# Optimization experiments

Hardware: AMD Instinct MI355X
Metric: run time of the kernel (lower is better)

## Reference

```python
import jax, jax.numpy as jnp
import numpy as np

ALPHA = 0.2          # LeakyReLU negative slope
NEG_BIG = -9e15      # mask value from the original code


def setup_inputs() -> dict:
    key = jax.random.key(0)
    k1, k2, k3, k4, k5 = jax.random.split(key, 5)
    N, Fin, Fout, C = 8192, 2048, 256, 8
    x = jax.random.normal(k1, (N, Fin), dtype=jnp.float32)
    # xavier_uniform-ish scale for params
    W = jax.random.normal(k2, (C, Fin, Fout), dtype=jnp.float32) / np.sqrt(Fin).astype(np.float32)
    a = jax.random.normal(k3, (2 * Fout, 1), dtype=jnp.float32) / np.sqrt(2 * Fout).astype(np.float32)
    cam_ids = jax.random.randint(k4, (N,), 0, C, dtype=jnp.int32)
    adj = jax.random.randint(k5, (N, N), 0, 2, dtype=jnp.int32)
    return {"x": x, "W": W, "a": a, "cam_ids": cam_ids, "adj": adj}


def reference(x, W, a, cam_ids, adj):
    N = x.shape[0]
    Fout = W.shape[-1]
    # per-node camera-specific projection: h[i] = x[i] @ W[cam_ids[i]]
    # compute all-camera projections (N, C, Fout) then gather per node;
    # avoids materializing W[cam_ids] of shape (N, Fin, Fout)
    hs = jnp.einsum('nd,cdo->nco', x, W)                       # (N, C, Fout)
    h = jnp.take_along_axis(hs, cam_ids[:, None, None], axis=1)[:, 0, :]  # (N, Fout)
    # e_ij = leakyrelu([h_i, h_j] @ a) = leakyrelu(h_i.a1 + h_j.a2)
    a1 = a[:Fout, 0]
    a2 = a[Fout:, 0]
    e = jax.nn.leaky_relu((h @ a1)[:, None] + (h @ a2)[None, :], ALPHA)  # (N, N)
    att = jnp.where(adj > 0, e, jnp.float32(NEG_BIG))
    att = jax.nn.softmax(att, axis=1)
    # dropout is identity at eval (p applied only in training)
    h_prime = att @ h                                          # (N, Fout)
    return jax.nn.elu(h_prime)                                 # concat=True -> ELU
```

## Files before the change

### kernel.cpp

```cpp
#include <hip/hip_runtime.h>

#define NR 8192
#define FIN 2048
#define FOUT 256
#define ALPHA 0.2f
#define NTMAX 136

typedef float f32x4 __attribute__((ext_vector_type(4)));
typedef float f32x16 __attribute__((ext_vector_type(16)));
typedef int i32x4 __attribute__((ext_vector_type(4)));
typedef unsigned int u32x4 __attribute__((ext_vector_type(4)));
typedef unsigned short u16x4 __attribute__((ext_vector_type(4)));
typedef unsigned short u16x8 __attribute__((ext_vector_type(8)));
typedef __bf16 bf16x8 __attribute__((ext_vector_type(8)));
typedef _Float16 f16x8 __attribute__((ext_vector_type(8)));
typedef _Float16 f16x4 __attribute__((ext_vector_type(4)));

__device__ __forceinline__ unsigned short f2bf(float f){
  unsigned u = __float_as_uint(f);
  return (unsigned short)((u + 0x7fffu + ((u >> 16) & 1u)) >> 16);
}
__device__ __forceinline__ float bf2f(unsigned short b){
  return __uint_as_float(((unsigned)b) << 16);
}

__device__ __forceinline__ void gload16(const void* gptr, void* lptr){
  __builtin_amdgcn_global_load_lds(
      (const __attribute__((address_space(1))) unsigned int*)gptr,
      (__attribute__((address_space(3))) unsigned int*)lptr, 16, 0, 0);
}

__global__ void k_bucket(const int* __restrict__ cam, int* __restrict__ rowlist,
                         int* __restrict__ tileCam, int* __restrict__ prows){
  __shared__ int cnt[256][8];
  __shared__ int base[8];
  __shared__ int scnt[8];
  __shared__ int tstart[9];
  __shared__ int tcL[NTMAX], tlocL[NTMAX];
  int t = threadIdx.x;
  int loc[8];
  #pragma unroll
  for (int c = 0; c < 8; c++) loc[c] = 0;
  for (int k = 0; k < 32; k++){ int n = t*32 + k; loc[cam[n] & 7]++; }
  #pragma unroll
  for (int c = 0; c < 8; c++) cnt[t][c] = loc[c];
  __syncthreads();
  if (t < 8){
    int s = 0;
    for (int i = 0; i < 256; i++){ int v = cnt[i][t]; cnt[i][t] = s; s += v; }
    scnt[t] = s;
  }
  __syncthreads();
  if (t == 0){
    int s = 0;
    for (int c = 0; c < 8; c++){ base[c] = s; s += scnt[c]; }
    int ts = 0;
    for (int c = 0; c < 8; c++){ tstart[c] = ts; ts += (scnt[c] + 63) >> 6; }
    tstart[8] = ts;
  }
  __syncthreads();
  int off[8];
  #pragma unroll
  for (int c = 0; c < 8; c++) off[c] = base[c] + cnt[t][c];
  for (int k = 0; k < 32; k++){
    int n = t*32 + k; int c = cam[n] & 7;
    rowlist[off[c]++] = n;
  }
  __syncthreads();
  if (t < NTMAX){
    int tc = -1, tl = 0;
    if (t < tstart[8]){
      for (int c = 0; c < 8; c++)
        if (t >= tstart[c] && t < tstart[c+1]){ tc = c; tl = t - tstart[c]; }
    }
    tcL[t] = tc; tlocL[t] = tl;
    tileCam[t] = tc;
  }
  __syncthreads();
  for (int s = t; s < NTMAX*64; s += 256){
    int tile = s >> 6;
    int c = tcL[tile];
    int v = -1;
    if (c >= 0){
      int li = tlocL[tile]*64 + (s & 63);
      if (li < scnt[c]) v = rowlist[base[c] + li];
    }
    prows[s] = v;
  }
}

__global__ __launch_bounds__(256) void k_wth(const float* __restrict__ W,
                                             _Float16* __restrict__ WhT){
  __shared__ _Float16 tl[64][72];
  int t = threadIdx.x;
  int k0 = blockIdx.x*64, n0 = blockIdx.y*64, c = blockIdx.z;
  {
    int kk = t >> 2, nq = (t & 3)*16;
    const float* src = W + ((size_t)c*FIN + k0 + kk)*FOUT + n0 + nq;
    #pragma unroll
    for (int q = 0; q < 4; q++){
      f32x4 v = *(const f32x4*)(src + q*4);
      #pragma unroll
      for (int e = 0; e < 4; e++) tl[nq + q*4 + e][kk] = (_Float16)v[e];
    }
  }
  __syncthreads();
  {
    int nn = t >> 2, kq = (t & 3)*16;
    union { u32x4 v[2]; _Float16 s[16]; } buf;
    #pragma unroll
    for (int e = 0; e < 16; e++) buf.s[e] = tl[nn][kq + e];
    u32x4* dst = (u32x4*)(WhT + ((size_t)c*FOUT + n0 + nn)*FIN + k0 + kq);
    dst[0] = buf.v[0]; dst[1] = buf.v[1];
  }
}

__global__ __launch_bounds__(256) void k_gmm(const float* __restrict__ x,
    const _Float16* __restrict__ WhT, const int* __restrict__ tileCam,
    const int* __restrict__ prows, float* __restrict__ partial, int klen){
  __shared__ _Float16 ab[2][10240];
  __shared__ int rows[64];
  __shared__ int growL[64];
  int tile = blockIdx.x;
  int cam = tileCam[tile];
  if (cam < 0) return;
  int t = threadIdx.x;
  if (t < 64){ int r = prows[tile*64 + t]; rows[t] = r; growL[t] = (r < 0) ? 0 : r; }
  __syncthreads();
  int ks = blockIdx.y;
  int k0 = ks * klen;
  int lane = t & 63, w = t >> 6;
  int wr = w >> 1, wc = w & 1;
  int rA = ((t >> 6) & 1)*32 + (t & 31);
  int koffA = (t >> 7)*16 + ((t >> 5) & 1)*8;
  const float* srcA = x + (size_t)growL[rA]*FIN + k0 + koffA;
  const _Float16* srcB[4];
  #pragma unroll
  for (int q = 0; q < 4; q++){
    int c2 = q*256 + t;
    int colg = ((c2 >> 6) & 7)*32 + (t & 31);
    srcB[q] = WhT + ((size_t)cam*FOUT + colg)*FIN + k0
            + (c2 >> 9)*16 + ((t >> 5) & 1)*8;
  }
  f32x16 acc[4];
  #pragma unroll
  for (int nb = 0; nb < 4; nb++)
    #pragma unroll
    for (int r = 0; r < 16; r++) acc[nb][r] = 0.f;

  int nsteps = klen >> 5;
  int cur = 0;
  {
    f32x4 a0 = *(const f32x4*)srcA;
    f32x4 a1 = *(const f32x4*)(srcA + 4);
    #pragma unroll
    for (int q = 0; q < 4; q++) gload16(srcB[q], &ab[0][2048 + (q*256 + t)*8]);
    f16x8 hv;
    #pragma unroll
    for (int e = 0; e < 4; e++){ hv[e] = (_Float16)a0[e]; hv[4+e] = (_Float16)a1[e]; }
    *(f16x8*)&ab[0][t*8] = hv;
  }
  __syncthreads();
  for (int s = 0; s < nsteps; s++){
    bool have = (s + 1 < nsteps);
    int adv = have ? (s + 1)*32 : 0;
    f32x4 na0 = *(const f32x4*)(srcA + adv);
    f32x4 na1 = *(const f32x4*)(srcA + adv + 4);
    if (have){
      #pragma unroll
      for (int q = 0; q < 4; q++)
        gload16(srcB[q] + adv, &ab[cur ^ 1][2048 + (q*256 + t)*8]);
    }
    const _Float16* base = ab[cur];
    f16x8 af[2]; f16x8 bfr[2][4];
    #pragma unroll
    for (int kk = 0; kk < 2; kk++){
      af[kk] = *(const f16x8*)(base + ((kk*2 + wr)*64 + lane)*8);
      #pragma unroll
      for (int nb = 0; nb < 4; nb++)
        bfr[kk][nb] = *(const f16x8*)(base + 2048 + ((kk*8 + wc*4 + nb)*64 + lane)*8);
    }
    #pragma unroll
    for (int kk = 0; kk < 2; kk++)
      #pragma unroll
      for (int nb = 0; nb < 4; nb++)
        acc[nb] = __builtin_amdgcn_mfma_f32_32x32x16_f16(af[kk], bfr[kk][nb], acc[nb], 0, 0, 0);
    if (have){
      f16x8 hv;
      #pragma unroll
      for (int e = 0; e < 4; e++){ hv[e] = (_Float16)na0[e]; hv[4+e] = (_Float16)na1[e]; }
      *(f16x8*)&ab[cur ^ 1][t*8] = hv;
    }
    __syncthreads();
    cur ^= 1;
  }
  int colb = wc*128;
  #pragma unroll
  for (int nb = 0; nb < 4; nb++){
    #pragma unroll
    for (int r = 0; r < 16; r++){
      int rowl = wr*32 + (r & 3) + 8*(r >> 2) + 4*(lane >> 5);
      int grow = rows[rowl];
      if (grow >= 0)
        partial[((size_t)ks*NR + grow)*FOUT + colb + nb*32 + (lane & 31)] = acc[nb][r];
    }
  }
}

__global__ __launch_bounds__(256) void k_hsum(const float* __restrict__ partial,
    const float* __restrict__ a, unsigned short* __restrict__ hbf,
    float* __restrict__ s1, float* __restrict__ s2, float* __restrict__ bm,
    int ksplit){
  __shared__ float a1l[FOUT], a2l[FOUT];
  __shared__ float smax[4];
  int t = threadIdx.x;
  a1l[t] = a[t]; a2l[t] = a[FOUT + t];
  __syncthreads();
  int w = t >> 6, lane = t & 63;
  int row = blockIdx.x*4 + w;
  f32x4 s; s[0] = s[1] = s[2] = s[3] = 0.f;
  for (int ks = 0; ks < ksplit; ks++)
    s += *(const f32x4*)(partial + ((size_t)ks*NR + row)*FOUT + lane*4);
  u16x4 pk;
  #pragma unroll
  for (int e = 0; e < 4; e++) pk[e] = f2bf(s[e]);
  *(u16x4*)(hbf + (size_t)row*FOUT + lane*4) = pk;
  f32x4 a1v = *(const f32x4*)&a1l[lane*4];
  f32x4 a2v = *(const f32x4*)&a2l[lane*4];
  float p1 = 0.f, p2 = 0.f;
  #pragma unroll
  for (int e = 0; e < 4; e++){ p1 = fmaf(s[e], a1v[e], p1); p2 = fmaf(s[e], a2v[e], p2); }
  #pragma unroll
  for (int off = 32; off > 0; off >>= 1){
    p1 += __shfl_xor(p1, off);
    p2 += __shfl_xor(p2, off);
  }
  if (lane == 0){ s1[row] = p1; s2[row] = p2; smax[w] = p2; }
  __syncthreads();
  if (t == 0)
    bm[blockIdx.x] = fmaxf(fmaxf(smax[0], smax[1]), fmaxf(smax[2], smax[3]));
}

__global__ void k_transpose(const unsigned short* __restrict__ in,
                            unsigned short* __restrict__ out){
  __shared__ unsigned short tl[64][72];
  int t = threadIdx.x;
  int j0 = blockIdx.x*64, c0 = blockIdx.y*64;
  {
    int jj = t >> 2, cq = (t & 3)*16;
    union { u32x4 v[2]; unsigned short s[16]; } buf;
    const u32x4* src = (const u32x4*)(in + (size_t)(j0 + jj)*FOUT + c0 + cq);
    buf.v[0] = src[0]; buf.v[1] = src[1];
    #pragma unroll
    for (int k = 0; k < 16; k++) tl[cq + k][jj] = buf.s[k];
  }
  __syncthreads();
  {
    int cc = t >> 2, jq = (t & 3)*16;
    union { u32x4 v[2]; unsigned short s[16]; } buf;
    #pragma unroll
    for (int k = 0; k < 16; k++) buf.s[k] = tl[cc][jq + k];
    u32x4* dst = (u32x4*)(out + (size_t)(c0 + cc)*NR + j0 + jq);
    dst[0] = buf.v[0]; dst[1] = buf.v[1];
  }
}

__global__ __launch_bounds__(512) void k_flash(const int* __restrict__ adj,
    const float* __restrict__ s1g, const float* __restrict__ s2g,
    const float* __restrict__ bm, const unsigned short* __restrict__ hT,
    float* __restrict__ hp, float* __restrict__ Dp, int jchunks){
  __shared__ unsigned short pl[64][72];
  __shared__ float s1l[64], ml[64], Dl[64], red[8];
  int t = threadIdx.x;
  int i0 = blockIdx.x*64;
  int jc = blockIdx.y;
  int nj = NR / jchunks;
  int jbase = jc * nj;
  int w = t >> 6, lane = t & 63;
  {
    float v = -3.0e38f;
    for (int k = t; k < NR/4; k += 512) v = fmaxf(v, bm[k]);
    #pragma unroll
    for (int off = 32; off > 0; off >>= 1) v = fmaxf(v, __shfl_xor(v, off));
    if (lane == 0) red[w] = v;
  }
  __syncthreads();
  if (t == 0){
    float v = red[0];
    #pragma unroll
    for (int k = 1; k < 8; k++) v = fmaxf(v, red[k]);
    red[0] = v;
  }
  __syncthreads();
  float maxS2 = red[0];
  if (t < 64){
    float sv = s1g[i0 + t];
    s1l[t] = sv;
    float mm = sv + maxS2;
    ml[t] = fmaxf(mm, ALPHA*mm);
  }
  __syncthreads();
  int il = t >> 3, tj = t & 7;
  float s1i = s1l[il], mi = ml[il];
  float Dacc = 0.f;
  f32x16 acc0, acc1;
  #pragma unroll
  for (int k = 0; k < 16; k++){ acc0[k] = 0.f; acc1[k] = 0.f; }
  const unsigned short* hTw = hT + (size_t)(w*32 + (lane & 31))*NR;
  const int* arow = adj + (size_t)(i0 + il)*NR + jbase + tj*8;
  i32x4 ad0 = __builtin_nontemporal_load((const i32x4*)arow);
  i32x4 ad1 = __builtin_nontemporal_load(((const i32x4*)arow) + 1);
  f32x4 s20 = *(const f32x4*)(s2g + jbase + tj*8);
  f32x4 s21 = *(const f32x4*)(s2g + jbase + tj*8 + 4);
  for (int jt = 0; jt < nj; jt += 64){
    int j0 = jbase + jt;
    i32x4 c0 = ad0, c1 = ad1;
    f32x4 t0 = s20, t1 = s21;
    if (jt + 64 < nj){
      arow += 64;
      ad0 = __builtin_nontemporal_load((const i32x4*)arow);
      ad1 = __builtin_nontemporal_load(((const i32x4*)arow) + 1);
      s20 = *(const f32x4*)(s2g + j0 + 64 + tj*8);
      s21 = *(const f32x4*)(s2g + j0 + 64 + tj*8 + 4);
    }
    u16x8 pu;
    float Dloc = 0.f;
    #pragma unroll
    for (int e = 0; e < 4; e++){
      float e0 = s1i + t0[e]; e0 = fmaxf(e0, ALPHA*e0);
      float p0 = (c0[e] > 0) ? __expf(e0 - mi) : 0.f;
      unsigned short b0 = f2bf(p0); pu[e] = b0; Dloc += bf2f(b0);
      float e1 = s1i + t1[e]; e1 = fmaxf(e1, ALPHA*e1);
      float p1 = (c1[e] > 0) ? __expf(e1 - mi) : 0.f;
      unsigned short b1 = f2bf(p1); pu[e + 4] = b1; Dloc += bf2f(b1);
    }
    Dacc += Dloc;
    bf16x8 bfr[4];
    #pragma unroll
    for (int ks = 0; ks < 4; ks++){
      int koff = ks*16 + (lane >> 5)*8;
      bfr[ks] = *(const bf16x8*)(hTw + j0 + koff);
    }
    *(u16x8*)&pl[il][tj*8] = pu;
    __syncthreads();
    #pragma unroll
    for (int ks = 0; ks < 4; ks++){
      int koff = ks*16 + (lane >> 5)*8;
      bf16x8 a0 = *(const bf16x8*)&pl[lane & 31][koff];
      acc0 = __builtin_amdgcn_mfma_f32_32x32x16_bf16(a0, bfr[ks], acc0, 0, 0, 0);
      bf16x8 a1 = *(const bf16x8*)&pl[32 + (lane & 31)][koff];
      acc1 = __builtin_amdgcn_mfma_f32_32x32x16_bf16(a1, bfr[ks], acc1, 0, 0, 0);
    }
    __syncthreads();
  }
  Dacc += __shfl_xor(Dacc, 1);
  Dacc += __shfl_xor(Dacc, 2);
  Dacc += __shfl_xor(Dacc, 4);
  if (tj == 0) Dl[il] = Dacc;
  __syncthreads();
  if (t < 64) Dp[(size_t)jc*NR + i0 + t] = Dl[t];
  float* hpb = hp + (size_t)jc*NR*FOUT;
  int col = w*32 + (lane & 31);
  #pragma unroll
  for (int r = 0; r < 16; r++){
    int rowl = (r & 3) + 8*(r >> 2) + 4*(lane >> 5);
    hpb[(size_t)(i0 + rowl)*FOUT + col] = acc0[r];
    hpb[(size_t)(i0 + 32 + rowl)*FOUT + col] = acc1[r];
  }
}

__global__ void k_final(const float* __restrict__ hp, const float* __restrict__ Dp,
                        float* __restrict__ out, int jchunks){
  int g = blockIdx.x*256 + threadIdx.x;
  int i = g >> 6, cg = (g & 63)*4;
  f32x4 s; s[0] = s[1] = s[2] = s[3] = 0.f;
  float D = 0.f;
  for (int jc = 0; jc < jchunks; jc++){
    f32x4 v = *(const f32x4*)(hp + ((size_t)jc*NR + i)*FOUT + cg);
    s += v;
    D += Dp[(size_t)jc*NR + i];
  }
  float inv = (D > 0.f) ? 1.f / D : 0.f;
  f32x4 o;
  #pragma unroll
  for (int e = 0; e < 4; e++){
    float v = s[e]*inv;
    o[e] = (v > 0.f) ? v : expm1f(v);
  }
  *(f32x4*)(out + (size_t)i*FOUT + cg) = o;
}

extern "C" void kernel_launch(void* const* d_in, const int* in_sizes, int n_in,
                              void* d_out, int out_size, void* d_ws, size_t ws_size,
                              hipStream_t stream){
  (void)in_sizes; (void)n_in; (void)out_size;
  const float* x   = (const float*)d_in[0];
  const float* W   = (const float*)d_in[1];
  const float* a   = (const float*)d_in[2];
  const int*   cam = (const int*)d_in[3];
  const int*   adj = (const int*)d_in[4];
  float* out = (float*)d_out;
  char* ws = (char*)d_ws;

  int KS = 4, JC = 4;
  for (;;){
    size_t need = 0;
    need += (size_t)NR*4 + 256;
    need += (size_t)NTMAX*4 + 256;
    need += (size_t)NTMAX*64*4 + 256;
    need += (size_t)8*FIN*FOUT*2 + 256;
    need += (size_t)NR*FOUT*2 + 256;
    need += (size_t)NR*FOUT*2 + 256;
    need += (size_t)NR*4*2 + 512;
    need += (size_t)(NR/4)*4 + 256;
    need += (size_t)JC*NR*4 + 256;
    size_t sh1 = (size_t)KS*NR*FOUT*4;
    size_t sh2 = (size_t)JC*NR*FOUT*4;
    need += (sh1 > sh2 ? sh1 : sh2) + 256;
    if (need <= ws_size || (KS == 1 && JC == 1)) break;
    if (KS > 1) KS >>= 1;
    if (JC > 1) JC >>= 1;
  }

  size_t off = 0;
  auto alloc = [&](size_t b) -> void* {
    void* p = ws + off; off = (off + b + 255) & ~(size_t)255; return p;
  };
  int* rowlist  = (int*)alloc((size_t)NR*4);
  int* tileCam  = (int*)alloc((size_t)NTMAX*4);
  int* prows    = (int*)alloc((size_t)NTMAX*64*4);
  _Float16* WhT = (_Float16*)alloc((size_t)8*FIN*FOUT*2);
  unsigned short* hbf = (unsigned short*)alloc((size_t)NR*FOUT*2);
  unsigned short* hT  = (unsigned short*)alloc((size_t)NR*FOUT*2);
  float* s1 = (float*)alloc((size_t)NR*4);
  float* s2 = (float*)alloc((size_t)NR*4);
  float* bm = (float*)alloc((size_t)(NR/4)*4);
  float* Dp = (float*)alloc((size_t)JC*NR*4);
  size_t sh1 = (size_t)KS*NR*FOUT*4;
  size_t sh2 = (size_t)JC*NR*FOUT*4;
  void* shared = alloc(sh1 > sh2 ? sh1 : sh2);
  float* partial = (float*)shared;
  float* hp      = (float*)shared;

  int klen = FIN / KS;

  hipLaunchKernelGGL(k_bucket, dim3(1), dim3(256), 0, stream,
                     cam, rowlist, tileCam, prows);
  hipLaunchKernelGGL(k_wth, dim3(FIN/64, FOUT/64, 8), dim3(256), 0, stream, W, WhT);
  hipLaunchKernelGGL(k_gmm, dim3(NTMAX, KS), dim3(256), 0, stream,
                     x, WhT, tileCam, prows, partial, klen);
  hipLaunchKernelGGL(k_hsum, dim3(NR/4), dim3(256), 0, stream,
                     partial, a, hbf, s1, s2, bm, KS);
  hipLaunchKernelGGL(k_transpose, dim3(NR/64, FOUT/64), dim3(256), 0, stream, hbf, hT);
  hipLaunchKernelGGL(k_flash, dim3(NR/64, JC), dim3(512), 0, stream,
                     adj, s1, s2, bm, hT, hp, Dp, JC);
  hipLaunchKernelGGL(k_final, dim3((NR*FOUT/4)/256), dim3(256), 0, stream,
                     hp, Dp, out, JC);
}
```

Measured before the change: 236.3 us.

## Fuse hsum with transpose, flash with final via cooperative grid sync

Several kernels are merged. Row summation now writes the transposed bf16 h directly, which drops the separate transpose kernel and the hbf buffer. The bucket kernel writes prows directly instead of going through a rowlist pass. Flash attention and the final normalisation/ELU run in one cooperative kernel separated by a grid sync, with JC fixed at 2 and a fallback to separate launches. Split sizes become compile-time constants; the trade-off is only 128 blocks for hsumT and the cost of the grid barrier.

Result: slower. 271.8 us (+15.0%).

```diff
diff --git a/kernel.cpp b/kernel.cpp
--- a/kernel.cpp
+++ b/kernel.cpp
@@ -1,10 +1,18 @@
 #include <hip/hip_runtime.h>
+#include <hip/hip_cooperative_groups.h>
+
+namespace cg = cooperative_groups;
 
 #define NR 8192
 #define FIN 2048
 #define FOUT 256
 #define ALPHA 0.2f
 #define NTMAX 136
+#define KS 4
+#define KLEN 512
+#define NSTEPS 16
+#define JC 2
+#define NJ 4096
 
 typedef float f32x4 __attribute__((ext_vector_type(4)));
 typedef float f32x16 __attribute__((ext_vector_type(16)));
@@ -14,7 +22,6 @@
 typedef unsigned short u16x8 __attribute__((ext_vector_type(8)));
 typedef __bf16 bf16x8 __attribute__((ext_vector_type(8)));
 typedef _Float16 f16x8 __attribute__((ext_vector_type(8)));
-typedef _Float16 f16x4 __attribute__((ext_vector_type(4)));
 
 __device__ __forceinline__ unsigned short f2bf(float f){
   unsigned u = __float_as_uint(f);
@@ -23,25 +30,54 @@
 __device__ __forceinline__ float bf2f(unsigned short b){
   return __uint_as_float(((unsigned)b) << 16);
 }
-
 __device__ __forceinline__ void gload16(const void* gptr, void* lptr){
   __builtin_amdgcn_global_load_lds(
       (const __attribute__((address_space(1))) unsigned int*)gptr,
       (__attribute__((address_space(3))) unsigned int*)lptr, 16, 0, 0);
 }
 
-__global__ void k_bucket(const int* __restrict__ cam, int* __restrict__ rowlist,
-                         int* __restrict__ tileCam, int* __restrict__ prows){
-  __shared__ int cnt[256][8];
-  __shared__ int base[8];
-  __shared__ int scnt[8];
-  __shared__ int tstart[9];
-  __shared__ int tcL[NTMAX], tlocL[NTMAX];
-  int t = threadIdx.x;
+__device__ __forceinline__ void phase_wth(int item, int t,
+    const float* __restrict__ W, _Float16* __restrict__ WhT, char* smem){
+  _Float16* tl = (_Float16*)smem;
+  int k0 = (item & 31) << 6;
+  int n0 = ((item >> 5) & 3) << 6;
+  int c = item >> 7;
+  {
+    int kk = t >> 2, nq = (t & 3)*16;
+    const float* src = W + ((size_t)c*FIN + k0 + kk)*FOUT + n0 + nq;
+    #pragma unroll
+    for (int q = 0; q < 4; q++){
+      f32x4 v = *(const f32x4*)(src + q*4);
+      #pragma unroll
+      for (int e = 0; e < 4; e++) tl[(nq + q*4 + e)*72 + kk] = (_Float16)v[e];
+    }
+  }
+  __syncthreads();
+  {
+    int nn = t >> 2, kq = (t & 3)*16;
+    union { u32x4 v[2]; _Float16 s[16]; } buf;
+    #pragma unroll
+    for (int e = 0; e < 16; e++) buf.s[e] = tl[nn*72 + kq + e];
+    u32x4* dst = (u32x4*)(WhT + ((size_t)c*FOUT + n0 + nn)*FIN + k0 + kq);
+    dst[0] = buf.v[0]; dst[1] = buf.v[1];
+  }
+}
+
+__global__ __launch_bounds__(256) void k_wth(const float* __restrict__ W,
+                                             _Float16* __restrict__ WhT){
+  extern __shared__ char smem[];
+  phase_wth(blockIdx.x, threadIdx.x, W, WhT, smem);
+}
+
+__device__ __forceinline__ void phase_bucket(int t, const int* __restrict__ cam,
+    int* __restrict__ prows, int* __restrict__ tileCam, char* smem){
+  int (*cnt)[8] = (int(*)[8])smem;
+  int* scnt = (int*)(smem + 8192);
+  int* tst  = (int*)(smem + 8224);
   int loc[8];
   #pragma unroll
   for (int c = 0; c < 8; c++) loc[c] = 0;
-  for (int k = 0; k < 32; k++){ int n = t*32 + k; loc[cam[n] & 7]++; }
+  for (int k = 0; k < 32; k++) loc[cam[t*32 + k] & 7]++;
   #pragma unroll
   for (int c = 0; c < 8; c++) cnt[t][c] = loc[c];
   __syncthreads();
@@ -52,84 +88,55 @@
   }
   __syncthreads();
   if (t == 0){
-    int s = 0;
-    for (int c = 0; c < 8; c++){ base[c] = s; s += scnt[c]; }
     int ts = 0;
-    for (int c = 0; c < 8; c++){ tstart[c] = ts; ts += (scnt[c] + 63) >> 6; }
-    tstart[8] = ts;
+    for (int c = 0; c < 8; c++){ tst[c] = ts; ts += (scnt[c] + 63) >> 6; }
+    tst[8] = ts;
+  }
+  __syncthreads();
+  for (int s = t; s < NTMAX*64; s += 256) prows[s] = -1;
+  if (t < NTMAX){
+    int tc = -1, te = tst[8];
+    if (t < te){
+      #pragma unroll
+      for (int c = 0; c < 8; c++)
+        if (t >= tst[c] && t < tst[c+1]) tc = c;
+    }
+    tileCam[t] = tc;
   }
   __syncthreads();
   int off[8];
   #pragma unroll
-  for (int c = 0; c < 8; c++) off[c] = base[c] + cnt[t][c];
+  for (int c = 0; c < 8; c++) off[c] = cnt[t][c];
   for (int k = 0; k < 32; k++){
     int n = t*32 + k; int c = cam[n] & 7;
-    rowlist[off[c]++] = n;
-  }
-  __syncthreads();
-  if (t < NTMAX){
-    int tc = -1, tl = 0;
-    if (t < tstart[8]){
-      for (int c = 0; c < 8; c++)
-        if (t >= tstart[c] && t < tstart[c+1]){ tc = c; tl = t - tstart[c]; }
-    }
-    tcL[t] = tc; tlocL[t] = tl;
-    tileCam[t] = tc;
-  }
-  __syncthreads();
-  for (int s = t; s < NTMAX*64; s += 256){
-    int tile = s >> 6;
-    int c = tcL[tile];
-    int v = -1;
-    if (c >= 0){
-      int li = tlocL[tile]*64 + (s & 63);
-      if (li < scnt[c]) v = rowlist[base[c] + li];
-    }
-    prows[s] = v;
-  }
-}
-
-__global__ __launch_bounds__(256) void k_wth(const float* __restrict__ W,
-                                             _Float16* __restrict__ WhT){
-  __shared__ _Float16 tl[64][72];
-  int t = threadIdx.x;
-  int k0 = blockIdx.x*64, n0 = blockIdx.y*64, c = blockIdx.z;
-  {
-    int kk = t >> 2, nq = (t & 3)*16;
-    const float* src = W + ((size_t)c*FIN + k0 + kk)*FOUT + n0 + nq;
-    #pragma unroll
-    for (int q = 0; q < 4; q++){
-      f32x4 v = *(const f32x4*)(src + q*4);
-      #pragma unroll
-      for (int e = 0; e < 4; e++) tl[nq + q*4 + e][kk] = (_Float16)v[e];
-    }
-  }
-  __syncthreads();
-  {
-    int nn = t >> 2, kq = (t & 3)*16;
-    union { u32x4 v[2]; _Float16 s[16]; } buf;
-    #pragma unroll
-    for (int e = 0; e < 16; e++) buf.s[e] = tl[nn][kq + e];
-    u32x4* dst = (u32x4*)(WhT + ((size_t)c*FOUT + n0 + nn)*FIN + k0 + kq);
-    dst[0] = buf.v[0]; dst[1] = buf.v[1];
-  }
-}
-
-__global__ __launch_bounds__(256) void k_gmm(const float* __restrict__ x,
-    const _Float16* __restrict__ WhT, const int* __restrict__ tileCam,
-    const int* __restrict__ prows, float* __restrict__ partial, int klen){
-  __shared__ _Float16 ab[2][10240];
-  __shared__ int rows[64];
-  __shared__ int growL[64];
-  int tile = blockIdx.x;
-  int cam = tileCam[tile];
-  if (cam < 0) return;
-  int t = threadIdx.x;
-  if (t < 64){ int r = prows[tile*64 + t]; rows[t] = r; growL[t] = (r < 0) ? 0 : r; }
-  __syncthreads();
-  int ks = blockIdx.y;
-  int k0 = ks * klen;
+    int slot = off[c]++;
+    prows[(tst[c] + (slot >> 6))*64 + (slot & 63)] = n;
+  }
+}
+
+__global__ void k_bucket(const int* __restrict__ cam, int* __restrict__ prows,
+                         int* __restrict__ tileCam){
+  extern __shared__ char smem[];
+  phase_bucket(threadIdx.x, cam, prows, tileCam, smem);
+}
+
+__device__ __forceinline__ void phase_gmm(int item, int t,
+    const float* __restrict__ x, const _Float16* __restrict__ WhT,
+    const int* __restrict__ tileCam, const int* __restrict__ prows,
+    float* __restrict__ partial, char* smem){
+  int tile = item >> 2, ks = item & 3;
+  int camc = tileCam[tile];
+  if (camc < 0) return;
+  _Float16* ab = (_Float16*)smem;
+  int* rows  = (int*)(smem + 40960);
+  int* growL = (int*)(smem + 41216);
+  if (t < 64){
+    int r = prows[tile*64 + t];
+    rows[t] = r; growL[t] = (r < 0) ? 0 : r;
+  }
+  __syncthreads();
   int lane = t & 63, w = t >> 6;
+  int k0 = ks * KLEN;
   int wr = w >> 1, wc = w & 1;
   int rA = ((t >> 6) & 1)*32 + (t & 31);
   int koffA = (t >> 7)*16 + ((t >> 5) & 1)*8;
@@ -139,7 +146,7 @@
   for (int q = 0; q < 4; q++){
     int c2 = q*256 + t;
     int colg = ((c2 >> 6) & 7)*32 + (t & 31);
-    srcB[q] = WhT + ((size_t)cam*FOUT + colg)*FIN + k0
+    srcB[q] = WhT + ((size_t)camc*FOUT + colg)*FIN + k0
             + (c2 >> 9)*16 + ((t >> 5) & 1)*8;
   }
   f32x16 acc[4];
@@ -147,31 +154,29 @@
   for (int nb = 0; nb < 4; nb++)
     #pragma unroll
     for (int r = 0; r < 16; r++) acc[nb][r] = 0.f;
-
-  int nsteps = klen >> 5;
   int cur = 0;
   {
     f32x4 a0 = *(const f32x4*)srcA;
     f32x4 a1 = *(const f32x4*)(srcA + 4);
     #pragma unroll
-    for (int q = 0; q < 4; q++) gload16(srcB[q], &ab[0][2048 + (q*256 + t)*8]);
+    for (int q = 0; q < 4; q++) gload16(srcB[q], &ab[2048 + (q*256 + t)*8]);
     f16x8 hv;
     #pragma unroll
     for (int e = 0; e < 4; e++){ hv[e] = (_Float16)a0[e]; hv[4+e] = (_Float16)a1[e]; }
-    *(f16x8*)&ab[0][t*8] = hv;
-  }
-  __syncthreads();
-  for (int s = 0; s < nsteps; s++){
-    bool have = (s + 1 < nsteps);
+    *(f16x8*)&ab[t*8] = hv;
+  }
+  __syncthreads();
+  for (int s = 0; s < NSTEPS; s++){
+    bool have = (s + 1 < NSTEPS);
     int adv = have ? (s + 1)*32 : 0;
     f32x4 na0 = *(const f32x4*)(srcA + adv);
     f32x4 na1 = *(const f32x4*)(srcA + adv + 4);
     if (have){
       #pragma unroll
       for (int q = 0; q < 4; q++)
-        gload16(srcB[q] + adv, &ab[cur ^ 1][2048 + (q*256 + t)*8]);
-    }
-    const _Float16* base = ab[cur];
+        gload16(srcB[q] + adv, &ab[(cur ^ 1)*10240 + 2048 + (q*256 + t)*8]);
+    }
+    const _Float16* base = ab + cur*10240;
     f16x8 af[2]; f16x8 bfr[2][4];
     #pragma unroll
     for (int kk = 0; kk < 2; kk++){
@@ -189,7 +194,7 @@
       f16x8 hv;
       #pragma unroll
       for (int e = 0; e < 4; e++){ hv[e] = (_Float16)na0[e]; hv[4+e] = (_Float16)na1[e]; }
-      *(f16x8*)&ab[cur ^ 1][t*8] = hv;
+      *(f16x8*)&ab[(cur ^ 1)*10240 + t*8] = hv;
     }
     __syncthreads();
     cur ^= 1;
@@ -207,79 +212,90 @@
   }
 }
 
-__global__ __launch_bounds__(256) void k_hsum(const float* __restrict__ partial,
-    const float* __restrict__ a, unsigned short* __restrict__ hbf,
+__global__ __launch_bounds__(256, 3) void k_gmm(const float* __restrict__ x,
+    const _Float16* __restrict__ WhT, const int* __restrict__ tileCam,
+    const int* __restrict__ prows, float* __restrict__ partial){
+  extern __shared__ char smem[];
+  phase_gmm(blockIdx.x, threadIdx.x, x, WhT, tileCam, prows, partial, smem);
+}
+
+__device__ __forceinline__ void phase_hsumT(int blk, int t,
+    const float* __restrict__ partial, const float* __restrict__ a,
     float* __restrict__ s1, float* __restrict__ s2, float* __restrict__ bm,
-    int ksplit){
-  __shared__ float a1l[FOUT], a2l[FOUT];
-  __shared__ float smax[4];
-  int t = threadIdx.x;
+    unsigned short* __restrict__ hT, char* smem){
+  unsigned short* sums = (unsigned short*)smem;
+  float* a1l = (float*)(smem + 33792);
+  float* a2l = (float*)(smem + 34816);
+  float* redv = (float*)(smem + 35840);
+  int w = t >> 6, lane = t & 63;
+  int r0 = blk*64;
   a1l[t] = a[t]; a2l[t] = a[FOUT + t];
   __syncthreads();
+  float bmax = -3.0e38f;
+  #pragma unroll
+  for (int rep = 0; rep < 16; rep++){
+    int row = rep*4 + w;
+    const float* pp = partial + (size_t)(r0 + row)*FOUT + lane*4;
+    f32x4 s; s[0] = s[1] = s[2] = s[3] = 0.f;
+    #pragma unroll
+    for (int ks = 0; ks < KS; ks++)
+      s += *(const f32x4*)(pp + (size_t)ks*NR*FOUT);
+    u16x4 pk;
+    #pragma unroll
+    for (int e = 0; e < 4; e++) pk[e] = f2bf(s[e]);
+    *(u16x4*)&sums[row*264 + lane*4] = pk;
+    f32x4 a1v = *(const f32x4*)&a1l[lane*4];
+    f32x4 a2v = *(const f32x4*)&a2l[lane*4];
+    float p1 = 0.f, p2 = 0.f;
+    #pragma unroll
+    for (int e = 0; e < 4; e++){ p1 = fmaf(s[e], a1v[e], p1); p2 = fmaf(s[e], a2v[e], p2); }
+    #pragma unroll
+    for (int off = 32; off > 0; off >>= 1){
+      p1 += __shfl_xor(p1, off);
+      p2 += __shfl_xor(p2, off);
+    }
+    if (lane == 0){
+      s1[r0 + row] = p1; s2[r0 + row] = p2;
+      bmax = fmaxf(bmax, p2);
+    }
+  }
+  if (lane == 0) redv[w] = bmax;
+  __syncthreads();
+  if (t == 0)
+    bm[blk] = fmaxf(fmaxf(redv[0], redv[1]), fmaxf(redv[2], redv[3]));
+  int c = t;
+  #pragma unroll
+  for (int q = 0; q < 8; q++){
+    u16x8 v;
+    #pragma unroll
+    for (int e = 0; e < 8; e++) v[e] = sums[(q*8 + e)*264 + c];
+    *(u16x8*)(hT + (size_t)c*NR + r0 + q*8) = v;
+  }
+}
+
+__global__ __launch_bounds__(256) void k_hsumT(const float* __restrict__ partial,
+    const float* __restrict__ a, float* __restrict__ s1, float* __restrict__ s2,
+    float* __restrict__ bm, unsigned short* __restrict__ hT){
+  extern __shared__ char smem[];
+  phase_hsumT(blockIdx.x, threadIdx.x, partial, a, s1, s2, bm, hT, smem);
+}
+
+__device__ __forceinline__ void phase_flash(int blk, int t,
+    const int* __restrict__ adj, const float* __restrict__ s1g,
+    const float* __restrict__ s2g, const float* __restrict__ bm,
+    const unsigned short* __restrict__ hT, float* __restrict__ hp,
+    float* __restrict__ Dp, char* smem){
+  unsigned short (*pl)[72] = (unsigned short(*)[72])smem;
+  float* s1l = (float*)(smem + 9216);
+  float* ml  = (float*)(smem + 9472);
+  float* Dl  = (float*)(smem + 9728);
+  float* red = (float*)(smem + 9984);
   int w = t >> 6, lane = t & 63;
-  int row = blockIdx.x*4 + w;
-  f32x4 s; s[0] = s[1] = s[2] = s[3] = 0.f;
-  for (int ks = 0; ks < ksplit; ks++)
-    s += *(const f32x4*)(partial + ((size_t)ks*NR + row)*FOUT + lane*4);
-  u16x4 pk;
-  #pragma unroll
-  for (int e = 0; e < 4; e++) pk[e] = f2bf(s[e]);
-  *(u16x4*)(hbf + (size_t)row*FOUT + lane*4) = pk;
-  f32x4 a1v = *(const f32x4*)&a1l[lane*4];
-  f32x4 a2v = *(const f32x4*)&a2l[lane*4];
-  float p1 = 0.f, p2 = 0.f;
-  #pragma unroll
-  for (int e = 0; e < 4; e++){ p1 = fmaf(s[e], a1v[e], p1); p2 = fmaf(s[e], a2v[e], p2); }
-  #pragma unroll
-  for (int off = 32; off > 0; off >>= 1){
-    p1 += __shfl_xor(p1, off);
-    p2 += __shfl_xor(p2, off);
-  }
-  if (lane == 0){ s1[row] = p1; s2[row] = p2; smax[w] = p2; }
-  __syncthreads();
-  if (t == 0)
-    bm[blockIdx.x] = fmaxf(fmaxf(smax[0], smax[1]), fmaxf(smax[2], smax[3]));
-}
-
-__global__ void k_transpose(const unsigned short* __restrict__ in,
-                            unsigned short* __restrict__ out){
-  __shared__ unsigned short tl[64][72];
-  int t = threadIdx.x;
-  int j0 = blockIdx.x*64, c0 = blockIdx.y*64;
+  int it = blk & 127, jc = blk >> 7;
+  int i0 = it*64;
+  int jbase = jc * NJ;
   {
-    int jj = t >> 2, cq = (t & 3)*16;
-    union { u32x4 v[2]; unsigned short s[16]; } buf;
-    const u32x4* src = (const u32x4*)(in + (size_t)(j0 + jj)*FOUT + c0 + cq);
-    buf.v[0] = src[0]; buf.v[1] = src[1];
-    #pragma unroll
-    for (int k = 0; k < 16; k++) tl[cq + k][jj] = buf.s[k];
-  }
-  __syncthreads();
-  {
-    int cc = t >> 2, jq = (t & 3)*16;
-    union { u32x4 v[2]; unsigned short s[16]; } buf;
-    #pragma unroll
-    for (int k = 0; k < 16; k++) buf.s[k] = tl[cc][jq + k];
-    u32x4* dst = (u32x4*)(out + (size_t)(c0 + cc)*NR + j0 + jq);
-    dst[0] = buf.v[0]; dst[1] = buf.v[1];
-  }
-}
-
-__global__ __launch_bounds__(512) void k_flash(const int* __restrict__ adj,
-    const float* __restrict__ s1g, const float* __restrict__ s2g,
-    const float* __restrict__ bm, const unsigned short* __restrict__ hT,
-    float* __restrict__ hp, float* __restrict__ Dp, int jchunks){
-  __shared__ unsigned short pl[64][72];
-  __shared__ float s1l[64], ml[64], Dl[64], red[8];
-  int t = threadIdx.x;
-  int i0 = blockIdx.x*64;
-  int jc = blockIdx.y;
-  int nj = NR / jchunks;
-  int jbase = jc * nj;
-  int w = t >> 6, lane = t & 63;
-  {
-    float v = -3.0e38f;
-    for (int k = t; k < NR/4; k += 512) v = fmaxf(v, bm[k]);
+    float v = (t < 128) ? bm[t] : -3.0e38f;
     #pragma unroll
     for (int off = 32; off > 0; off >>= 1) v = fmaxf(v, __shfl_xor(v, off));
     if (lane == 0) red[w] = v;
@@ -312,11 +328,11 @@
   i32x4 ad1 = __builtin_nontemporal_load(((const i32x4*)arow) + 1);
   f32x4 s20 = *(const f32x4*)(s2g + jbase + tj*8);
   f32x4 s21 = *(const f32x4*)(s2g + jbase + tj*8 + 4);
-  for (int jt = 0; jt < nj; jt += 64){
+  for (int jt = 0; jt < NJ; jt += 64){
     int j0 = jbase + jt;
     i32x4 c0 = ad0, c1 = ad1;
     f32x4 t0 = s20, t1 = s21;
-    if (jt + 64 < nj){
+    if (jt + 64 < NJ){
       arow += 64;
       ad0 = __builtin_nontemporal_load((const i32x4*)arow);
       ad1 = __builtin_nontemporal_load(((const i32x4*)arow) + 1);
@@ -369,31 +385,55 @@
   }
 }
 
-__global__ void k_final(const float* __restrict__ hp, const float* __restrict__ Dp,
-                        float* __restrict__ out, int jchunks){
-  int g = blockIdx.x*256 + threadIdx.x;
-  int i = g >> 6, cg = (g & 63)*4;
-  f32x4 s; s[0] = s[1] = s[2] = s[3] = 0.f;
-  float D = 0.f;
-  for (int jc = 0; jc < jchunks; jc++){
-    f32x4 v = *(const f32x4*)(hp + ((size_t)jc*NR + i)*FOUT + cg);
-    s += v;
-    D += Dp[(size_t)jc*NR + i];
-  }
-  float inv = (D > 0.f) ? 1.f / D : 0.f;
-  f32x4 o;
-  #pragma unroll
-  for (int e = 0; e < 4; e++){
-    float v = s[e]*inv;
-    o[e] = (v > 0.f) ? v : expm1f(v);
-  }
-  *(f32x4*)(out + (size_t)i*FOUT + cg) = o;
+__device__ __forceinline__ void phase_final(int gid,
+    const float* __restrict__ hp, const float* __restrict__ Dp,
+    float* __restrict__ out){
+  #pragma unroll
+  for (int rep = 0; rep < 4; rep++){
+    int u = rep*131072 + gid;
+    int i = u >> 6, cg4 = (u & 63)*4;
+    f32x4 s = *(const f32x4*)(hp + (size_t)i*FOUT + cg4);
+    s += *(const f32x4*)(hp + (size_t)(NR + i)*FOUT + cg4);
+    float D = Dp[i] + Dp[NR + i];
+    float inv = (D > 0.f) ? 1.f / D : 0.f;
+    f32x4 o;
+    #pragma unroll
+    for (int e = 0; e < 4; e++){
+      float v = s[e]*inv;
+      o[e] = (v > 0.f) ? v : expm1f(v);
+    }
+    *(f32x4*)(out + (size_t)i*FOUT + cg4) = o;
+  }
+}
+
+__global__ __launch_bounds__(512, 2) void k_flash(const int* __restrict__ adj,
+    const float* __restrict__ s1, const float* __restrict__ s2,
+    const float* __restrict__ bm, const unsigned short* __restrict__ hT,
+    float* __restrict__ hp, float* __restrict__ Dp){
+  extern __shared__ char smem[];
+  phase_flash(blockIdx.x, threadIdx.x, adj, s1, s2, bm, hT, hp, Dp, smem);
+}
+
+__global__ __launch_bounds__(256) void k_final(const float* __restrict__ hp,
+    const float* __restrict__ Dp, float* __restrict__ out){
+  phase_final(blockIdx.x*256 + threadIdx.x, hp, Dp, out);
+}
+
+__global__ __launch_bounds__(512, 2) void kB2(const int* __restrict__ adj,
+    const float* __restrict__ s1, const float* __restrict__ s2,
+    const float* __restrict__ bm, const unsigned short* __restrict__ hT,
+    float* __restrict__ hp, float* __restrict__ Dp, float* __restrict__ out){
+  extern __shared__ char smem[];
+  cg::grid_group grid = cg::this_grid();
+  phase_flash(blockIdx.x, threadIdx.x, adj, s1, s2, bm, hT, hp, Dp, smem);
+  grid.sync();
+  phase_final(blockIdx.x*512 + threadIdx.x, hp, Dp, out);
 }
 
 extern "C" void kernel_launch(void* const* d_in, const int* in_sizes, int n_in,
                               void* d_out, int out_size, void* d_ws, size_t ws_size,
                               hipStream_t stream){
-  (void)in_sizes; (void)n_in; (void)out_size;
+  (void)in_sizes; (void)n_in; (void)out_size; (void)ws_size;
   const float* x   = (const float*)d_in[0];
   const float* W   = (const float*)d_in[1];
   const float* a   = (const float*)d_in[2];
@@ -402,58 +442,38 @@
   float* out = (float*)d_out;
   char* ws = (char*)d_ws;
 
-  int KS = 4, JC = 4;
-  for (;;){
-    size_t need = 0;
-    need += (size_t)NR*4 + 256;
-    need += (size_t)NTMAX*4 + 256;
-    need += (size_t)NTMAX*64*4 + 256;
-    need += (size_t)8*FIN*FOUT*2 + 256;
-    need += (size_t)NR*FOUT*2 + 256;
-    need += (size_t)NR*FOUT*2 + 256;
-    need += (size_t)NR*4*2 + 512;
-    need += (size_t)(NR/4)*4 + 256;
-    need += (size_t)JC*NR*4 + 256;
-    size_t sh1 = (size_t)KS*NR*FOUT*4;
-    size_t sh2 = (size_t)JC*NR*FOUT*4;
-    need += (sh1 > sh2 ? sh1 : sh2) + 256;
-    if (need <= ws_size || (KS == 1 && JC == 1)) break;
-    if (KS > 1) KS >>= 1;
-    if (JC > 1) JC >>= 1;
-  }
-
   size_t off = 0;
   auto alloc = [&](size_t b) -> void* {
     void* p = ws + off; off = (off + b + 255) & ~(size_t)255; return p;
   };
-  int* rowlist  = (int*)alloc((size_t)NR*4);
   int* tileCam  = (int*)alloc((size_t)NTMAX*4);
   int* prows    = (int*)alloc((size_t)NTMAX*64*4);
   _Float16* WhT = (_Float16*)alloc((size_t)8*FIN*FOUT*2);
-  unsigned short* hbf = (unsigned short*)alloc((size_t)NR*FOUT*2);
-  unsigned short* hT  = (unsigned short*)alloc((size_t)NR*FOUT*2);
+  unsigned short* hT = (unsigned short*)alloc((size_t)NR*FOUT*2);
   float* s1 = (float*)alloc((size_t)NR*4);
   float* s2 = (float*)alloc((size_t)NR*4);
-  float* bm = (float*)alloc((size_t)(NR/4)*4);
+  float* bm = (float*)alloc(128*4);
   float* Dp = (float*)alloc((size_t)JC*NR*4);
-  size_t sh1 = (size_t)KS*NR*FOUT*4;
-  size_t sh2 = (size_t)JC*NR*FOUT*4;
-  void* shared = alloc(sh1 > sh2 ? sh1 : sh2);
-  float* partial = (float*)shared;
-  float* hp      = (float*)shared;
-
-  int klen = FIN / KS;
-
-  hipLaunchKernelGGL(k_bucket, dim3(1), dim3(256), 0, stream,
-                     cam, rowlist, tileCam, prows);
-  hipLaunchKernelGGL(k_wth, dim3(FIN/64, FOUT/64, 8), dim3(256), 0, stream, W, WhT);
-  hipLaunchKernelGGL(k_gmm, dim3(NTMAX, KS), dim3(256), 0, stream,
-                     x, WhT, tileCam, prows, partial, klen);
-  hipLaunchKernelGGL(k_hsum, dim3(NR/4), dim3(256), 0, stream,
-                     partial, a, hbf, s1, s2, bm, KS);
-  hipLaunchKernelGGL(k_transpose, dim3(NR/64, FOUT/64), dim3(256), 0, stream, hbf, hT);
-  hipLaunchKernelGGL(k_flash, dim3(NR/64, JC), dim3(512), 0, stream,
-                     adj, s1, s2, bm, hT, hp, Dp, JC);
-  hipLaunchKernelGGL(k_final, dim3((NR*FOUT/4)/256), dim3(256), 0, stream,
-                     hp, Dp, out, JC);
-}
+  float* partial = (float*)alloc((size_t)KS*NR*FOUT*4);
+  float* hp = partial;
+
+  hipLaunchKernelGGL(k_wth, dim3(1024), dim3(256), 9216, stream, W, WhT);
+  hipLaunchKernelGGL(k_bucket, dim3(1), dim3(256), 8448, stream,
+                     cam, prows, tileCam);
+  hipLaunchKernelGGL(k_gmm, dim3(NTMAX*4), dim3(256), 41728, stream,
+                     x, WhT, tileCam, prows, partial);
+  hipLaunchKernelGGL(k_hsumT, dim3(128), dim3(256), 36096, stream,
+                     partial, a, s1, s2, bm, hT);
+  {
+    void* args[] = { (void*)&adj, (void*)&s1, (void*)&s2, (void*)&bm,
+                     (void*)&hT, (void*)&hp, (void*)&Dp, (void*)&out };
+    hipError_t rc = hipLaunchCooperativeKernel((const void*)kB2, dim3(256),
+                                               dim3(512), args, 10240, stream);
+    if (rc != hipSuccess){
+      hipLaunchKernelGGL(k_flash, dim3(256), dim3(512), 10240, stream,
+                         adj, s1, s2, bm, hT, hp, Dp);
+      hipLaunchKernelGGL(k_final, dim3(512), dim3(256), 0, stream,
+                         hp, Dp, out);
+    }
+  }
+}
```
